# Kernel tuning notes

Hardware: AMD Instinct MI355X
Metric: run time of the kernel (lower is better)

Reference implementation:

```python
import jax, jax.numpy as jnp
import numpy as np
from jax import lax

# Model constants (match init_kwargs)
DIM = 512
NUM_HEADS = 8
HEAD_DIM = 64
INNER = NUM_HEADS * HEAD_DIM  # 512
SCALE = HEAD_DIM ** -0.5
# CoaT ConvRelPosEnc window dict {3:2, 5:3, 7:3}: head-group sizes and kernel sizes
HEAD_SPLITS = [2, 3, 3]
KSIZES = [3, 5, 7]


def _depthwise_conv(x, w, b):
    # x: [B, Cg, H, W], w: [Cg, 1, k, k] (OIHW, depthwise), b: [Cg]
    cg = x.shape[1]
    y = lax.conv_general_dilated(
        x, w, window_strides=(1, 1), padding='SAME',
        feature_group_count=cg,
        dimension_numbers=('NCHW', 'OIHW', 'NCHW'))
    return y + b[None, :, None, None]


def setup_inputs() -> dict:
    key = jax.random.key(0)
    ks = jax.random.split(key, 10)
    B, Himg, Wimg = 16, 56, 56
    N = Himg * Wimg
    x = jax.random.normal(ks[0], (B, N, DIM), dtype=jnp.float32)
    w_qkv = jax.random.normal(ks[1], (3 * INNER, DIM), dtype=jnp.float32) * 0.02
    w_proj = jax.random.normal(ks[2], (DIM, INNER), dtype=jnp.float32) * 0.02
    b_proj = jnp.zeros((DIM,), dtype=jnp.float32)
    # depthwise conv params per head group: channels = split * HEAD_DIM
    w3 = jax.random.normal(ks[3], (2 * HEAD_DIM, 1, 3, 3), dtype=jnp.float32) * 0.02
    b3 = jnp.zeros((2 * HEAD_DIM,), dtype=jnp.float32)
    w5 = jax.random.normal(ks[4], (3 * HEAD_DIM, 1, 5, 5), dtype=jnp.float32) * 0.02
    b5 = jnp.zeros((3 * HEAD_DIM,), dtype=jnp.float32)
    w7 = jax.random.normal(ks[5], (3 * HEAD_DIM, 1, 7, 7), dtype=jnp.float32) * 0.02
    b7 = jnp.zeros((3 * HEAD_DIM,), dtype=jnp.float32)
    return {"x": x, "H": Himg, "W": Wimg,
            "w_qkv": w_qkv, "w_proj": w_proj, "b_proj": b_proj,
            "w3": w3, "b3": b3, "w5": w5, "b5": b5, "w7": w7, "b7": b7}


def reference(x, H, W, w_qkv, w_proj, b_proj, w3, b3, w5, b5, w7, b7):
    B, N, C = x.shape
    h, d = NUM_HEADS, HEAD_DIM
    qkv = x @ w_qkv.T  # [B, N, 3*INNER]
    q, k, v = jnp.split(qkv, 3, axis=-1)
    # b n (h d) -> b h n d
    def to_heads(t):
        return t.reshape(B, N, h, d).transpose(0, 2, 1, 3)
    q, k, v = to_heads(q), to_heads(k), to_heads(v)
    # factorized attention: softmax(k) over sequence dim, then two batched GEMMs
    k_softmax = jax.nn.softmax(k, axis=2)
    kv = jnp.einsum('bhnk,bhnv->bhkv', k_softmax, v)          # [B,h,d,d]
    factor_att = jnp.einsum('bhnk,bhkv->bhnv', q, kv)          # [B,h,N,d]
    # ConvRelPosEnc: depthwise conv on v (as 2D map), elementwise multiply by q
    v_img = v.transpose(0, 1, 3, 2).reshape(B, h * d, H, W)    # [B, h*d, H, W]
    c0, c1 = HEAD_SPLITS[0] * d, (HEAD_SPLITS[0] + HEAD_SPLITS[1]) * d
    conv_v = jnp.concatenate([
        _depthwise_conv(v_img[:, :c0], w3, b3),
        _depthwise_conv(v_img[:, c0:c1], w5, b5),
        _depthwise_conv(v_img[:, c1:], w7, b7),
    ], axis=1)                                                 # [B, h*d, H, W]
    conv_v = conv_v.reshape(B, h, d, N).transpose(0, 1, 3, 2)  # [B,h,N,d]
    crpe = q * conv_v
    out = SCALE * factor_att + crpe                            # [B,h,N,d]
    out = out.transpose(0, 2, 1, 3).reshape(B, N, h * d)       # b h n d -> b n (h d)
    out = out @ w_proj.T + b_proj
    return out
```

## Files before the change

### kernel.cpp

```cpp
#include <hip/hip_runtime.h>
#include <hip/hip_bf16.h>
#include <cstdint>
#include <cstddef>

using u16 = unsigned short;
using u32 = unsigned int;
using f32x4 = __attribute__((ext_vector_type(4))) float;
using bf16x8 = __attribute__((ext_vector_type(8))) short;

#define NB   16
#define NSEQ 3136
#define NH   8
#define HD   64
#define CDIM 512
#define CQKV 1536

static __device__ __forceinline__ u16 f2bf(float f) {
  u32 u = __builtin_bit_cast(u32, f);
  u = (u + 0x7FFFu + ((u >> 16) & 1u)) >> 16;
  return (u16)u;
}
static __device__ __forceinline__ float bf2f(u16 h) {
  u32 u = ((u32)h) << 16;
  return __builtin_bit_cast(float, u);
}
static __device__ __forceinline__ void async16(const void* g, void* l) {
  __builtin_amdgcn_global_load_lds((const __attribute__((address_space(1))) u32*)g,
                                   (__attribute__((address_space(3))) u32*)l, 16, 0, 0);
}

__global__ __launch_bounds__(256) void cvt_kernel(const float* __restrict__ in,
                                                  u16* __restrict__ out, int n4) {
  int i = (int)(blockIdx.x * 256 + threadIdx.x);
  if (i >= n4) return;
  f32x4 v = *(const f32x4*)(in + (size_t)i * 4);
  uint2 uu;
  uu.x = (u32)f2bf(v[0]) | ((u32)f2bf(v[1]) << 16);
  uu.y = (u32)f2bf(v[2]) | ((u32)f2bf(v[3]) << 16);
  *(uint2*)(out + (size_t)i * 4) = uu;
}

#define VMW(n) asm volatile("s_waitcnt vmcnt(" #n ")" ::: "memory")

template<bool OUT_FP32>
__global__ __launch_bounds__(512, 2) void gemm256(
    const u16* __restrict__ Ap, const u16* __restrict__ Bp, void* __restrict__ Cp,
    const float* __restrict__ bias, int K, int lda, int ldb, int ldc, int nbn)
{
  __shared__ u16 sm[2][2][2][128 * 64];
  int nwg = (int)gridDim.x;
  int bid = (int)blockIdx.x;
  int wg = (bid & 7) * (nwg >> 3) + (bid >> 3);
  int bm = wg / nbn, bn = wg - bm * nbn;
  int m0 = bm * 256, n0 = bn * 256;
  int t = (int)threadIdx.x;
  int lane = t & 63, w = t >> 6;
  int wm = w >> 2, wn = w & 3;
  int lr = lane & 15, lk = (lane >> 4) * 8;

  f32x4 acc[2][2][4][2] = {};
  bf16x8 av[4][2], bv[2][2];
  const int KT = K >> 6;

  auto stage = [&](int b, int op, int half, int kt) {
    const u16* P = op ? Bp : Ap;
    int ld = op ? ldb : lda;
    int base0 = op ? n0 : m0;
    int gc = (kt << 6) + ((((t & 7) ^ ((t >> 3) & 7))) << 3);
    #pragma unroll
    for (int rd = 0; rd < 2; ++rd) {
      int gr = base0 + half * 128 + rd * 64 + (t >> 3);
      async16(P + (size_t)gr * ld + gc, &sm[b][op][half][rd * 4096 + w * 512]);
    }
  };
  auto LOADA = [&](int b, int h) {
    #pragma unroll
    for (int mi = 0; mi < 4; ++mi)
      #pragma unroll
      for (int kk = 0; kk < 2; ++kk) {
        int r = wm * 64 + mi * 16 + lr;
        int c = kk * 32 + lk;
        av[mi][kk] = *(const bf16x8*)&sm[b][0][h][r * 64 + (c ^ ((r & 7) << 3))];
      }
  };
  auto LOADB = [&](int b, int g) {
    #pragma unroll
    for (int ni = 0; ni < 2; ++ni)
      #pragma unroll
      for (int kk = 0; kk < 2; ++kk) {
        int r = wn * 32 + ni * 16 + lr;
        int c = kk * 32 + lk;
        bv[ni][kk] = *(const bf16x8*)&sm[b][1][g][r * 64 + (c ^ ((r & 7) << 3))];
      }
  };

#define BARSEQ                                                  \
  __builtin_amdgcn_s_barrier();                                 \
  asm volatile("s_waitcnt lgkmcnt(0)" ::: "memory");            \
  __builtin_amdgcn_sched_barrier(0);                            \
  __builtin_amdgcn_s_setprio(1)
#define ENDP                                                    \
  __builtin_amdgcn_s_setprio(0);                                \
  __builtin_amdgcn_s_barrier()
#define MMQ(h_, g_)                                                          \
  _Pragma("unroll")                                                          \
  for (int kk = 0; kk < 2; ++kk) {                                           \
    _Pragma("unroll")                                                        \
    for (int mi = 0; mi < 4; ++mi) {                                         \
      _Pragma("unroll")                                                      \
      for (int ni = 0; ni < 2; ++ni)                                         \
        acc[h_][g_][mi][ni] = __builtin_amdgcn_mfma_f32_16x16x32_bf16(       \
            av[mi][kk], bv[ni][kk], acc[h_][g_][mi][ni], 0, 0, 0);           \
    }                                                                        \
  }

  stage(0, 0, 0, 0); stage(0, 1, 0, 0); stage(0, 0, 1, 0); stage(0, 1, 1, 0);
  VMW(4);
  __builtin_amdgcn_s_barrier();

  for (int kt = 0; kt < KT - 1; ++kt) {
    int bb = kt & 1;
    LOADA(bb, 0); LOADB(bb, 0);
    stage(bb ^ 1, 0, 0, kt + 1);
    VMW(2);
    BARSEQ; MMQ(0, 0); ENDP;
    LOADB(bb, 1);
    stage(bb ^ 1, 1, 0, kt + 1);
    BARSEQ; MMQ(0, 1); ENDP;
    LOADA(bb, 1);
    stage(bb ^ 1, 0, 1, kt + 1);
    BARSEQ; MMQ(1, 1); ENDP;
    LOADB(bb, 0);
    stage(bb ^ 1, 1, 1, kt + 1);
    VMW(4);
    BARSEQ; MMQ(1, 0); ENDP;
  }
  {
    int bb = (KT - 1) & 1;
    LOADA(bb, 0); LOADB(bb, 0);
    VMW(0);
    BARSEQ; MMQ(0, 0); ENDP;
    LOADB(bb, 1);
    BARSEQ; MMQ(0, 1); ENDP;
    LOADA(bb, 1);
    BARSEQ; MMQ(1, 1); ENDP;
    LOADB(bb, 0);
    BARSEQ; MMQ(1, 0); ENDP;
  }
#undef MMQ
#undef BARSEQ
#undef ENDP

  if constexpr (!OUT_FP32) {
    __syncthreads();
    u16* cs = (u16*)sm;
    #pragma unroll
    for (int h = 0; h < 2; ++h)
      #pragma unroll
      for (int g = 0; g < 2; ++g)
        #pragma unroll
        for (int mi = 0; mi < 4; ++mi)
          #pragma unroll
          for (int ni = 0; ni < 2; ++ni)
            #pragma unroll
            for (int r = 0; r < 4; ++r) {
              int row = h * 128 + wm * 64 + mi * 16 + (lane >> 4) * 4 + r;
              int col = g * 128 + wn * 32 + ni * 16 + lr;
              cs[row * 256 + (col ^ (((row >> 2) & 7) << 3))] = f2bf(acc[h][g][mi][ni][r]);
            }
    __syncthreads();
    #pragma unroll
    for (int i = 0; i < 16; ++i) {
      int e = (i * 512 + t) * 8;
      int row = e >> 8, col = e & 255;
      uint4 v = *(const uint4*)&cs[row * 256 + (col ^ (((row >> 2) & 7) << 3))];
      *(uint4*)&((u16*)Cp)[(size_t)(m0 + row) * ldc + n0 + col] = v;
    }
  } else {
    float* cf = (float*)sm;
    #pragma unroll
    for (int h = 0; h < 2; ++h) {
      __syncthreads();
      #pragma unroll
      for (int g = 0; g < 2; ++g)
        #pragma unroll
        for (int mi = 0; mi < 4; ++mi)
          #pragma unroll
          for (int ni = 0; ni < 2; ++ni)
            #pragma unroll
            for (int r = 0; r < 4; ++r) {
              int row = wm * 64 + mi * 16 + (lane >> 4) * 4 + r;
              int col = g * 128 + wn * 32 + ni * 16 + lr;
              cf[row * 256 + (col ^ (((row >> 2) & 7) << 3))] = acc[h][g][mi][ni][r];
            }
      __syncthreads();
      #pragma unroll
      for (int i = 0; i < 16; ++i) {
        int e = (i * 512 + t) * 4;
        int row = e >> 8, col = e & 255;
        f32x4 v = *(const f32x4*)&cf[row * 256 + (col ^ (((row >> 2) & 7) << 3))];
        f32x4 b4 = *(const f32x4*)&bias[n0 + col];
        v += b4;
        *(f32x4*)&((float*)Cp)[(size_t)(m0 + h * 128 + row) * ldc + n0 + col] = v;
      }
    }
  }
}


static __device__ __forceinline__ void kvp_body(int bid, char* smem,
    const u16* __restrict__ qkvb, float* __restrict__ part) {
  int ns = bid & 7, h = (bid >> 3) & 7, b = bid >> 6;
  int t = (int)threadIdx.x;
  int lane = t & 63, w = t >> 6;
  u16* ekT = (u16*)smem;
  u16* vT  = (u16*)(smem + 8192);
  int nbase = ns * 392;
  int lr = lane & 15, lg = lane >> 4;
  f32x4 acc[4] = {};
  float sacc = 0.f;

  for (int tile = 0; tile < 7; ++tile) {
    __syncthreads();
    int lim = 392 - tile * 64;
    #pragma unroll
    for (int it = 0; it < 2; ++it) {
      int idx = it * 256 + t;
      int n = idx >> 3, c8 = idx & 7;
      uint4 kq; kq.x = 0u; kq.y = 0u; kq.z = 0u; kq.w = 0u;
      uint4 vq = kq;
      bool ok = (n < lim);
      if (ok) {
        size_t go = (size_t)(b * NSEQ + nbase + tile * 64 + n) * CQKV + h * HD + c8 * 8;
        kq = *(const uint4*)&qkvb[go + CDIM];
        vq = *(const uint4*)&qkvb[go + 2 * CDIM];
      }
      const u16* kp = (const u16*)&kq;
      const u16* vp = (const u16*)&vq;
      int pc = n ^ (c8 << 3);
      #pragma unroll
      for (int j = 0; j < 8; ++j) {
        int d = c8 * 8 + j;
        ekT[d * 64 + pc] = ok ? f2bf(__expf(bf2f(kp[j]))) : (u16)0;
        vT [d * 64 + pc] = vp[j];
      }
    }
    __syncthreads();
    bf16x8 av[2], bv[4][2];
    #pragma unroll
    for (int kk = 0; kk < 2; ++kk) {
      int r = w * 16 + lr;
      int c = kk * 32 + lg * 8;
      av[kk] = *(const bf16x8*)&ekT[r * 64 + (c ^ (((r >> 3) & 7) << 3))];
    }
    #pragma unroll
    for (int ni = 0; ni < 4; ++ni)
      #pragma unroll
      for (int kk = 0; kk < 2; ++kk) {
        int r = ni * 16 + lr;
        int c = kk * 32 + lg * 8;
        bv[ni][kk] = *(const bf16x8*)&vT[r * 64 + (c ^ (((r >> 3) & 7) << 3))];
      }
    #pragma unroll
    for (int kk = 0; kk < 2; ++kk)
      #pragma unroll
      for (int ni = 0; ni < 4; ++ni)
        acc[ni] = __builtin_amdgcn_mfma_f32_16x16x32_bf16(av[kk], bv[ni][kk], acc[ni], 0, 0, 0);
    {
      int r = w * 16 + lr;
      int c0 = lg * 16;
      int sw = (((r >> 3) & 7) << 3);
      bf16x8 s0 = *(const bf16x8*)&ekT[r * 64 + (c0 ^ sw)];
      bf16x8 s1 = *(const bf16x8*)&ekT[r * 64 + ((c0 + 8) ^ sw)];
      float ss = 0.f;
      #pragma unroll
      for (int j = 0; j < 8; ++j) ss += bf2f((u16)s0[j]) + bf2f((u16)s1[j]);
      sacc += ss;
    }
  }
  sacc += __shfl_xor(sacc, 16, 64);
  sacc += __shfl_xor(sacc, 32, 64);
  float* dst = part + (size_t)((ns * 16 + b) * 8 + h) * 4160;
  #pragma unroll
  for (int ni = 0; ni < 4; ++ni)
    #pragma unroll
    for (int r = 0; r < 4; ++r)
      dst[(w * 16 + lg * 4 + r) * 64 + ni * 16 + lr] = acc[ni][r];
  if (lane < 16) dst[4096 + w * 16 + lane] = sacc;
}

template<int R>
static __device__ __forceinline__ void conv_body(int bid, char* smem,
    const u16* __restrict__ qkvb, u16* __restrict__ cvout,
    const float* __restrict__ wp, const float* __restrict__ bias, int hbase, int nh) {
  constexpr int KS = 2 * R + 1;
  constexpr int WTY = 8 + 2 * R;
  constexpr int WTX = 14 + 2 * R;
  u16* vt = (u16*)smem;
  int hh = bid % nh;
  int tile = (bid / nh) % 28;
  int b = bid / (nh * 28);
  int h = hbase + hh;
  int y0 = (tile >> 2) * 8, x0 = (tile & 3) * 14;
  int t = (int)threadIdx.x;
  for (int idx = t; idx < WTY * WTX * 8; idx += 256) {
    int pix = idx >> 3, c8 = idx & 7;
    int py = pix / WTX, px = pix - py * WTX;
    int gy = y0 + py - R, gx = x0 + px - R;
    uint4 val; val.x = 0u; val.y = 0u; val.z = 0u; val.w = 0u;
    if (gy >= 0 && gy < 56 && gx >= 0 && gx < 56)
      val = *(const uint4*)&qkvb[(size_t)(b * NSEQ + gy * 56 + gx) * CQKV + 2 * CDIM + h * HD + c8 * 8];
    *(uint4*)&vt[pix * 64 + c8 * 8] = val;
  }
  __syncthreads();
  int d = t & 63, g = t >> 6;
  int cg = hh * 64 + d;
  float wr[KS * KS];
  #pragma unroll
  for (int i = 0; i < KS * KS; ++i) wr[i] = wp[cg * KS * KS + i];
  float bb = bias[cg];
  for (int px = g; px < 14; px += 4) {
    float acc[8];
    #pragma unroll
    for (int i = 0; i < 8; ++i) acc[i] = bb;
    #pragma unroll
    for (int iy = 0; iy < WTY; ++iy) {
      float val[KS];
      #pragma unroll
      for (int dx = 0; dx < KS; ++dx) val[dx] = bf2f(vt[(iy * WTX + px + dx) * 64 + d]);
      #pragma unroll
      for (int dy = 0; dy < KS; ++dy) {
        int py = iy - dy;
        if (py >= 0 && py < 8) {
          #pragma unroll
          for (int dx = 0; dx < KS; ++dx) acc[py] += wr[dy * KS + dx] * val[dx];
        }
      }
    }
    #pragma unroll
    for (int py = 0; py < 8; ++py)
      cvout[(size_t)(b * NSEQ + (y0 + py) * 56 + x0 + px) * CDIM + h * HD + d] = f2bf(acc[py]);
  }
}

__global__ __launch_bounds__(256) void mid_kernel(const u16* __restrict__ qkvb,
    u16* __restrict__ cvout, float* __restrict__ part,
    const float* __restrict__ w3, const float* __restrict__ b3,
    const float* __restrict__ w5, const float* __restrict__ b5,
    const float* __restrict__ w7, const float* __restrict__ b7) {
  __shared__ alignas(16) char smem[35840];
  int bid = (int)blockIdx.x;
  int q9 = bid / 9, r9 = bid - q9 * 9;
  if (r9 == 0 || r9 == 4) {
    kvp_body(q9 * 2 + (r9 == 4 ? 1 : 0), smem, qkvb, part);
  } else {
    int s = (r9 < 4) ? (r9 - 1) : (r9 - 2);
    int cid = q9 * 7 + s;
    if (cid < 896)        conv_body<1>(cid,        smem, qkvb, cvout, w3, b3, 0, 2);
    else if (cid < 2240)  conv_body<2>(cid - 896,  smem, qkvb, cvout, w5, b5, 2, 3);
    else                  conv_body<3>(cid - 2240, smem, qkvb, cvout, w7, b7, 5, 3);
  }
}

__global__ __launch_bounds__(256) void kv_reduce_kernel(const float* __restrict__ part,
                                                        float* __restrict__ kvb) {
  int idx = (int)(blockIdx.x * 256 + threadIdx.x);
  int bh = idx >> 10, e4 = idx & 1023;
  int b = bh >> 3, h = bh & 7;
  int dk = e4 >> 4;
  float s = 0.f;
  f32x4 o; o[0] = 0.f; o[1] = 0.f; o[2] = 0.f; o[3] = 0.f;
  #pragma unroll
  for (int c = 0; c < 8; ++c) {
    const float* src = part + (size_t)((c * 16 + b) * 8 + h) * 4160;
    o += *(const f32x4*)&src[e4 * 4];
    s += src[4096 + dk];
  }
  float inv = 1.0f / s;
  o *= inv;
  *(f32x4*)&kvb[(size_t)bh * 4096 + e4 * 4] = o;
}

__global__ __launch_bounds__(256) void combine_kernel(u16* __restrict__ qkvb,
                                                      const u16* __restrict__ cvin,
                                                      const float* __restrict__ kvb) {
  int bid = (int)blockIdx.x;
  int rt = bid % 49;
  int h = (bid / 49) & 7;
  int b = bid / 392;
  int n0 = rt * 64;
  int t = (int)threadIdx.x;
  int lane = t & 63, w = t >> 6;
  __shared__ u16 qs[64 * 72];
  __shared__ u16 cvs[64 * 64];
  __shared__ u16 kvT[64 * 64];

  #pragma unroll
  for (int i = 0; i < 2; ++i) {
    int idx = i * 256 + t;
    int row = idx >> 3, c8 = idx & 7;
    int srccol = (c8 ^ (row & 7)) << 3;
    async16(qkvb + (size_t)(b * NSEQ + n0 + row) * CQKV + h * HD + srccol, &qs[idx * 8]);
    async16(cvin + (size_t)(b * NSEQ + n0 + row) * CDIM + h * HD + srccol, &cvs[idx * 8]);
  }
  const float* kvsrc = kvb + (size_t)(b * 8 + h) * 4096;
  #pragma unroll
  for (int i = 0; i < 4; ++i) {
    int idx = i * 256 + t;
    int dk = idx & 63, dv0 = (idx >> 6) * 4;
    f32x4 v = *(const f32x4*)&kvsrc[dk * 64 + dv0];
    #pragma unroll
    for (int j = 0; j < 4; ++j) {
      int dv = dv0 + j;
      kvT[dv * 64 + ((((dk >> 3) ^ (dv & 7)) << 3) | (dk & 7))] = f2bf(v[j]);
    }
  }
  VMW(0);
  __syncthreads();

  int lr = lane & 15, lk = (lane >> 4) * 8;
  f32x4 acc[4] = {};
  bf16x8 av[2], bv[4][2];
  #pragma unroll
  for (int kk = 0; kk < 2; ++kk) {
    int r = w * 16 + lr;
    int c = kk * 32 + lk;
    av[kk] = *(const bf16x8*)&qs[r * 64 + (c ^ ((r & 7) << 3))];
  }
  #pragma unroll
  for (int ni = 0; ni < 4; ++ni)
    #pragma unroll
    for (int kk = 0; kk < 2; ++kk) {
      int r = ni * 16 + lr;
      int c = kk * 32 + lk;
      bv[ni][kk] = *(const bf16x8*)&kvT[r * 64 + (c ^ ((r & 7) << 3))];
    }
  #pragma unroll
  for (int kk = 0; kk < 2; ++kk)
    #pragma unroll
    for (int ni = 0; ni < 4; ++ni)
      acc[ni] = __builtin_amdgcn_mfma_f32_16x16x32_bf16(av[kk], bv[ni][kk], acc[ni], 0, 0, 0);

  float outv[4][4];
  #pragma unroll
  for (int ni = 0; ni < 4; ++ni)
    #pragma unroll
    for (int r = 0; r < 4; ++r) {
      int nrow = w * 16 + (lane >> 4) * 4 + r;
      int dv = ni * 16 + lr;
      int sw = ((((dv >> 3) ^ (nrow & 7)) << 3) | (dv & 7));
      float qv = bf2f(qs[nrow * 64 + sw]);
      float cv = bf2f(cvs[nrow * 64 + sw]);
      outv[ni][r] = 0.125f * acc[ni][r] + qv * cv;
    }
  __syncthreads();
  #pragma unroll
  for (int ni = 0; ni < 4; ++ni)
    #pragma unroll
    for (int r = 0; r < 4; ++r) {
      int nrow = w * 16 + (lane >> 4) * 4 + r;
      int dv = ni * 16 + lr;
      qs[nrow * 72 + dv] = f2bf(outv[ni][r]);
    }
  __syncthreads();
  {
    int row = t >> 2, c0 = (t & 3) * 16;
    uint4 x0 = *(const uint4*)&qs[row * 72 + c0];
    uint4 x1 = *(const uint4*)&qs[row * 72 + c0 + 8];
    u16* dst = &qkvb[(size_t)(b * NSEQ + n0 + row) * CQKV + h * HD + c0];
    *(uint4*)dst = x0;
    *(uint4*)&dst[8] = x1;
  }
}

extern "C" void kernel_launch(void* const* d_in, const int* in_sizes, int n_in,
                              void* d_out, int out_size, void* d_ws, size_t ws_size,
                              hipStream_t stream) {
  (void)in_sizes; (void)n_in; (void)out_size; (void)ws_size;
  const float* x      = (const float*)d_in[0];
  const float* w_qkv  = (const float*)d_in[3];
  const float* w_proj = (const float*)d_in[4];
  const float* b_proj = (const float*)d_in[5];
  const float* w3 = (const float*)d_in[6];
  const float* b3 = (const float*)d_in[7];
  const float* w5 = (const float*)d_in[8];
  const float* b5 = (const float*)d_in[9];
  const float* w7 = (const float*)d_in[10];
  const float* b7 = (const float*)d_in[11];
  float* out = (float*)d_out;

  char* ws = (char*)d_ws;
  u16* qkvb = (u16*)ws;        ws += (size_t)50176 * 1536 * 2;
  u16* wqb  = (u16*)ws;        ws += (size_t)1536 * 512 * 2;
  u16* wpb  = (u16*)ws;        ws += (size_t)512 * 512 * 2;
  float* kvpart = (float*)ws;  ws += (size_t)1024 * 4160 * 4;
  float* kvb = (float*)ws;     ws += (size_t)16 * 8 * 64 * 64 * 4;
  u16* xb = (u16*)ws;          ws += (size_t)50176 * 512 * 2;

  cvt_kernel<<<768, 256, 0, stream>>>(w_qkv, wqb, 1536 * 512 / 4);
  cvt_kernel<<<256, 256, 0, stream>>>(w_proj, wpb, 512 * 512 / 4);
  cvt_kernel<<<25088, 256, 0, stream>>>(x, xb, 50176 * 512 / 4);
  gemm256<false><<<1176, 512, 0, stream>>>(xb, wqb, qkvb, nullptr,
                                           512, 512, 512, 1536, 6);
  mid_kernel<<<4608, 256, 0, stream>>>(qkvb, xb, kvpart, w3, b3, w5, b5, w7, b7);
  kv_reduce_kernel<<<512, 256, 0, stream>>>(kvpart, kvb);
  combine_kernel<<<6272, 256, 0, stream>>>(qkvb, xb, kvb);
  gemm256<true><<<392, 512, 0, stream>>>(qkvb, wpb, out, b_proj,
                                         512, 1536, 512, 512, 2);
}
```

Before: 285.4 us.

## Transpose conv tile to channel-major shared layout and compute 2x14 outputs per thread

The depthwise-conv stage now stores the V tile in shared memory channel-major with padded rows (22 u16 per row), so each thread reads contiguous pixel rows for its channel as packed 32-bit pairs. Each thread now computes two output rows by fourteen columns, sharing every loaded input row between both output rows, where before it computed one column by eight rows. This cuts LDS reads and bf16 conversions per FMA. In exchange the scattered 2-byte LDS writes during the tile load may cause bank conflicts, register pressure rises from 28 accumulators plus up to 49 weights, and the shared buffer grows, which may lower occupancy.

```diff
diff --git a/kernel.cpp b/kernel.cpp
--- a/kernel.cpp
+++ b/kernel.cpp
@@ -296,6 +296,8 @@
   constexpr int KS = 2 * R + 1;
   constexpr int WTY = 8 + 2 * R;
   constexpr int WTX = 14 + 2 * R;
+  constexpr int RPAD = 22;
+  constexpr int ROWS = (R == 2) ? 13 : WTY;
   u16* vt = (u16*)smem;
   int hh = bid % nh;
   int tile = (bid / nh) % 28;
@@ -310,36 +312,58 @@
     uint4 val; val.x = 0u; val.y = 0u; val.z = 0u; val.w = 0u;
     if (gy >= 0 && gy < 56 && gx >= 0 && gx < 56)
       val = *(const uint4*)&qkvb[(size_t)(b * NSEQ + gy * 56 + gx) * CQKV + 2 * CDIM + h * HD + c8 * 8];
-    *(uint4*)&vt[pix * 64 + c8 * 8] = val;
+    const u16* vp = (const u16*)&val;
+    #pragma unroll
+    for (int j = 0; j < 8; ++j)
+      vt[(c8 * 8 + j) * (ROWS * RPAD) + py * RPAD + px] = vp[j];
   }
   __syncthreads();
   int d = t & 63, g = t >> 6;
   int cg = hh * 64 + d;
-  float wr[KS * KS];
-  #pragma unroll
-  for (int i = 0; i < KS * KS; ++i) wr[i] = wp[cg * KS * KS + i];
+  float w[KS * KS];
+  #pragma unroll
+  for (int i = 0; i < KS * KS; ++i) w[i] = wp[cg * KS * KS + i];
   float bb = bias[cg];
-  for (int px = g; px < 14; px += 4) {
-    float acc[8];
-    #pragma unroll
-    for (int i = 0; i < 8; ++i) acc[i] = bb;
-    #pragma unroll
-    for (int iy = 0; iy < WTY; ++iy) {
-      float val[KS];
-      #pragma unroll
-      for (int dx = 0; dx < KS; ++dx) val[dx] = bf2f(vt[(iy * WTX + px + dx) * 64 + d]);
-      #pragma unroll
-      for (int dy = 0; dy < KS; ++dy) {
-        int py = iy - dy;
-        if (py >= 0 && py < 8) {
-          #pragma unroll
-          for (int dx = 0; dx < KS; ++dx) acc[py] += wr[dy * KS + dx] * val[dx];
-        }
-      }
-    }
-    #pragma unroll
-    for (int py = 0; py < 8; ++py)
-      cvout[(size_t)(b * NSEQ + (y0 + py) * 56 + x0 + px) * CDIM + h * HD + d] = f2bf(acc[py]);
+  float acc[2][14];
+  #pragma unroll
+  for (int pp = 0; pp < 2; ++pp)
+    #pragma unroll
+    for (int px = 0; px < 14; ++px) acc[pp][px] = bb;
+  const u16* rowbase = &vt[d * (ROWS * RPAD)];
+  int py0 = g * 2;
+  #pragma unroll
+  for (int dy2 = 0; dy2 <= KS; ++dy2) {
+    float val[WTX];
+    const u32* rp = (const u32*)&rowbase[(py0 + dy2) * RPAD];
+    #pragma unroll
+    for (int c = 0; c < WTX / 2; ++c) {
+      u32 u = rp[c];
+      val[2 * c]     = __builtin_bit_cast(float, u << 16);
+      val[2 * c + 1] = __builtin_bit_cast(float, u & 0xffff0000u);
+    }
+    if (dy2 < KS) {
+      #pragma unroll
+      for (int dx = 0; dx < KS; ++dx) {
+        float wv = w[dy2 * KS + dx];
+        #pragma unroll
+        for (int px = 0; px < 14; ++px) acc[0][px] += wv * val[px + dx];
+      }
+    }
+    if (dy2 >= 1) {
+      #pragma unroll
+      for (int dx = 0; dx < KS; ++dx) {
+        float wv = w[(dy2 - 1) * KS + dx];
+        #pragma unroll
+        for (int px = 0; px < 14; ++px) acc[1][px] += wv * val[px + dx];
+      }
+    }
+  }
+  #pragma unroll
+  for (int pp = 0; pp < 2; ++pp) {
+    int py = py0 + pp;
+    #pragma unroll
+    for (int px = 0; px < 14; ++px)
+      cvout[(size_t)(b * NSEQ + (y0 + py) * 56 + x0 + px) * CDIM + h * HD + d] = f2bf(acc[pp][px]);
   }
 }
 
@@ -348,7 +372,7 @@
     const float* __restrict__ w3, const float* __restrict__ b3,
     const float* __restrict__ w5, const float* __restrict__ b5,
     const float* __restrict__ w7, const float* __restrict__ b7) {
-  __shared__ alignas(16) char smem[35840];
+  __shared__ alignas(16) char smem[39424];
   int bid = (int)blockIdx.x;
   int q9 = bid / 9, r9 = bid - q9 * 9;
   if (r9 == 0 || r9 == 4) {
```

Measured after the change: 296.7 us. 1.04x slower.

## Make QKV GEMM persistent and prefetch next tile during epilogue

Applied to the files above, without the earlier changes.

The QKV projection GEMM becomes a persistent kernel. A 256-block grid loops over all 1176 output tiles. During the last K step of each tile it stages the first K slice of the next tile into the free shared-memory buffer. It then writes the bf16 epilogue through the other buffer in two halves, so the prefetch overlaps the store. The goal is to hide per-tile prologue and launch tail cost, at the expense of running only one block per CU and uneven tile counts per block.

```diff
diff --git a/kernel.cpp b/kernel.cpp
--- a/kernel.cpp
+++ b/kernel.cpp
@@ -28,6 +28,11 @@
   __builtin_amdgcn_global_load_lds((const __attribute__((address_space(1))) u32*)g,
                                    (__attribute__((address_space(3))) u32*)l, 16, 0, 0);
 }
+
+#define VMW(n) asm volatile("s_waitcnt vmcnt(" #n ")" ::: "memory")
+#define LGKM0BAR                                                \
+  asm volatile("s_waitcnt lgkmcnt(0)" ::: "memory");            \
+  __builtin_amdgcn_s_barrier()
 
 __global__ __launch_bounds__(256) void cvt_kernel(const float* __restrict__ in,
                                                   u16* __restrict__ out, int n4) {
@@ -40,32 +45,26 @@
   *(uint2*)(out + (size_t)i * 4) = uu;
 }
 
-#define VMW(n) asm volatile("s_waitcnt vmcnt(" #n ")" ::: "memory")
-
 template<bool OUT_FP32>
 __global__ __launch_bounds__(512, 2) void gemm256(
     const u16* __restrict__ Ap, const u16* __restrict__ Bp, void* __restrict__ Cp,
-    const float* __restrict__ bias, int K, int lda, int ldb, int ldc, int nbn)
+    const float* __restrict__ bias, int K, int lda, int ldb, int ldc, int nbn, int ntotal)
 {
   __shared__ u16 sm[2][2][2][128 * 64];
-  int nwg = (int)gridDim.x;
-  int bid = (int)blockIdx.x;
-  int wg = (bid & 7) * (nwg >> 3) + (bid >> 3);
-  int bm = wg / nbn, bn = wg - bm * nbn;
-  int m0 = bm * 256, n0 = bn * 256;
   int t = (int)threadIdx.x;
   int lane = t & 63, w = t >> 6;
   int wm = w >> 2, wn = w & 3;
   int lr = lane & 15, lk = (lane >> 4) * 8;
-
-  f32x4 acc[2][2][4][2] = {};
+  const int KT = K >> 6;
+  int grid = (int)gridDim.x;
+  int nper = ntotal >> 3;
+
   bf16x8 av[4][2], bv[2][2];
-  const int KT = K >> 6;
-
-  auto stage = [&](int b, int op, int half, int kt) {
+
+  auto stage = [&](int b, int op, int half, int kt, int bm0, int bn0) {
     const u16* P = op ? Bp : Ap;
     int ld = op ? ldb : lda;
-    int base0 = op ? n0 : m0;
+    int base0 = op ? bn0 : bm0;
     int gc = (kt << 6) + ((((t & 7) ^ ((t >> 3) & 7))) << 3);
     #pragma unroll
     for (int rd = 0; rd < 2; ++rd) {
@@ -93,6 +92,27 @@
         bv[ni][kk] = *(const bf16x8*)&sm[b][1][g][r * 64 + (c ^ ((r & 7) << 3))];
       }
   };
+
+  int raw = (int)blockIdx.x;
+  int wg = (raw & 7) * nper + (raw >> 3);
+  int bm = wg / nbn, bn = wg - bm * nbn;
+  int m0 = bm * 256, n0 = bn * 256;
+
+  stage(0, 0, 0, 0, m0, n0); stage(0, 1, 0, 0, m0, n0);
+  stage(0, 0, 1, 0, m0, n0); stage(0, 1, 1, 0, m0, n0);
+  VMW(4);
+  __builtin_amdgcn_s_barrier();
+
+  while (true) {
+    f32x4 acc[2][2][4][2] = {};
+    int nraw = raw + grid;
+    bool has_next = (nraw < ntotal);
+    int nm0 = 0, nn0 = 0;
+    if (has_next) {
+      int nwg2 = (nraw & 7) * nper + (nraw >> 3);
+      int nbm = nwg2 / nbn, nbn2 = nwg2 - nbm * nbn;
+      nm0 = nbm * 256; nn0 = nbn2 * 256;
+    }
 
 #define BARSEQ                                                  \
   __builtin_amdgcn_s_barrier();                                 \
@@ -114,96 +134,114 @@
     }                                                                        \
   }
 
-  stage(0, 0, 0, 0); stage(0, 1, 0, 0); stage(0, 0, 1, 0); stage(0, 1, 1, 0);
-  VMW(4);
-  __builtin_amdgcn_s_barrier();
-
-  for (int kt = 0; kt < KT - 1; ++kt) {
-    int bb = kt & 1;
-    LOADA(bb, 0); LOADB(bb, 0);
-    stage(bb ^ 1, 0, 0, kt + 1);
-    VMW(2);
-    BARSEQ; MMQ(0, 0); ENDP;
-    LOADB(bb, 1);
-    stage(bb ^ 1, 1, 0, kt + 1);
-    BARSEQ; MMQ(0, 1); ENDP;
-    LOADA(bb, 1);
-    stage(bb ^ 1, 0, 1, kt + 1);
-    BARSEQ; MMQ(1, 1); ENDP;
-    LOADB(bb, 0);
-    stage(bb ^ 1, 1, 1, kt + 1);
-    VMW(4);
-    BARSEQ; MMQ(1, 0); ENDP;
-  }
-  {
-    int bb = (KT - 1) & 1;
-    LOADA(bb, 0); LOADB(bb, 0);
-    VMW(0);
-    BARSEQ; MMQ(0, 0); ENDP;
-    LOADB(bb, 1);
-    BARSEQ; MMQ(0, 1); ENDP;
-    LOADA(bb, 1);
-    BARSEQ; MMQ(1, 1); ENDP;
-    LOADB(bb, 0);
-    BARSEQ; MMQ(1, 0); ENDP;
-  }
+    for (int kt = 0; kt < KT - 1; ++kt) {
+      int bb = kt & 1;
+      LOADA(bb, 0); LOADB(bb, 0);
+      stage(bb ^ 1, 0, 0, kt + 1, m0, n0);
+      VMW(2);
+      BARSEQ; MMQ(0, 0); ENDP;
+      LOADB(bb, 1);
+      stage(bb ^ 1, 1, 0, kt + 1, m0, n0);
+      BARSEQ; MMQ(0, 1); ENDP;
+      LOADA(bb, 1);
+      stage(bb ^ 1, 0, 1, kt + 1, m0, n0);
+      BARSEQ; MMQ(1, 1); ENDP;
+      LOADB(bb, 0);
+      stage(bb ^ 1, 1, 1, kt + 1, m0, n0);
+      VMW(4);
+      BARSEQ; MMQ(1, 0); ENDP;
+    }
+    {
+      int bb = (KT - 1) & 1;
+      if (has_next) {
+        LOADA(bb, 0); LOADB(bb, 0);
+        stage(bb ^ 1, 0, 0, 0, nm0, nn0);
+        VMW(2);
+        BARSEQ; MMQ(0, 0); ENDP;
+        LOADB(bb, 1);
+        stage(bb ^ 1, 1, 0, 0, nm0, nn0);
+        BARSEQ; MMQ(0, 1); ENDP;
+        LOADA(bb, 1);
+        stage(bb ^ 1, 0, 1, 0, nm0, nn0);
+        BARSEQ; MMQ(1, 1); ENDP;
+        LOADB(bb, 0);
+        stage(bb ^ 1, 1, 1, 0, nm0, nn0);
+        VMW(4);
+        BARSEQ; MMQ(1, 0); ENDP;
+      } else {
+        LOADA(bb, 0); LOADB(bb, 0);
+        VMW(0);
+        BARSEQ; MMQ(0, 0); ENDP;
+        LOADB(bb, 1);
+        BARSEQ; MMQ(0, 1); ENDP;
+        LOADA(bb, 1);
+        BARSEQ; MMQ(1, 1); ENDP;
+        LOADB(bb, 0);
+        BARSEQ; MMQ(1, 0); ENDP;
+      }
+    }
 #undef MMQ
 #undef BARSEQ
 #undef ENDP
 
-  if constexpr (!OUT_FP32) {
-    __syncthreads();
-    u16* cs = (u16*)sm;
-    #pragma unroll
-    for (int h = 0; h < 2; ++h)
-      #pragma unroll
-      for (int g = 0; g < 2; ++g)
+    if constexpr (!OUT_FP32) {
+      u16* cs = (u16*)&sm[1][0][0][0];
+      #pragma unroll
+      for (int h = 0; h < 2; ++h) {
+        LGKM0BAR;
         #pragma unroll
-        for (int mi = 0; mi < 4; ++mi)
+        for (int g = 0; g < 2; ++g)
           #pragma unroll
-          for (int ni = 0; ni < 2; ++ni)
+          for (int mi = 0; mi < 4; ++mi)
             #pragma unroll
-            for (int r = 0; r < 4; ++r) {
-              int row = h * 128 + wm * 64 + mi * 16 + (lane >> 4) * 4 + r;
-              int col = g * 128 + wn * 32 + ni * 16 + lr;
-              cs[row * 256 + (col ^ (((row >> 2) & 7) << 3))] = f2bf(acc[h][g][mi][ni][r]);
-            }
-    __syncthreads();
-    #pragma unroll
-    for (int i = 0; i < 16; ++i) {
-      int e = (i * 512 + t) * 8;
-      int row = e >> 8, col = e & 255;
-      uint4 v = *(const uint4*)&cs[row * 256 + (col ^ (((row >> 2) & 7) << 3))];
-      *(uint4*)&((u16*)Cp)[(size_t)(m0 + row) * ldc + n0 + col] = v;
-    }
-  } else {
-    float* cf = (float*)sm;
-    #pragma unroll
-    for (int h = 0; h < 2; ++h) {
-      __syncthreads();
-      #pragma unroll
-      for (int g = 0; g < 2; ++g)
+            for (int ni = 0; ni < 2; ++ni)
+              #pragma unroll
+              for (int r = 0; r < 4; ++r) {
+                int row = wm * 64 + mi * 16 + (lane >> 4) * 4 + r;
+                int col = g * 128 + wn * 32 + ni * 16 + lr;
+                cs[row * 256 + (col ^ (((row >> 2) & 7) << 3))] = f2bf(acc[h][g][mi][ni][r]);
+              }
+        LGKM0BAR;
         #pragma unroll
-        for (int mi = 0; mi < 4; ++mi)
+        for (int i = 0; i < 8; ++i) {
+          int e = (i * 512 + t) * 8;
+          int row = e >> 8, col = e & 255;
+          uint4 v = *(const uint4*)&cs[row * 256 + (col ^ (((row >> 2) & 7) << 3))];
+          *(uint4*)&((u16*)Cp)[(size_t)(m0 + h * 128 + row) * ldc + n0 + col] = v;
+        }
+      }
+    } else {
+      float* cf = (float*)sm;
+      #pragma unroll
+      for (int h = 0; h < 2; ++h) {
+        LGKM0BAR;
+        #pragma unroll
+        for (int g = 0; g < 2; ++g)
           #pragma unroll
-          for (int ni = 0; ni < 2; ++ni)
+          for (int mi = 0; mi < 4; ++mi)
             #pragma unroll
-            for (int r = 0; r < 4; ++r) {
-              int row = wm * 64 + mi * 16 + (lane >> 4) * 4 + r;
-              int col = g * 128 + wn * 32 + ni * 16 + lr;
-              cf[row * 256 + (col ^ (((row >> 2) & 7) << 3))] = acc[h][g][mi][ni][r];
-            }
-      __syncthreads();
-      #pragma unroll
-      for (int i = 0; i < 16; ++i) {
-        int e = (i * 512 + t) * 4;
-        int row = e >> 8, col = e & 255;
-        f32x4 v = *(const f32x4*)&cf[row * 256 + (col ^ (((row >> 2) & 7) << 3))];
-        f32x4 b4 = *(const f32x4*)&bias[n0 + col];
-        v += b4;
-        *(f32x4*)&((float*)Cp)[(size_t)(m0 + h * 128 + row) * ldc + n0 + col] = v;
-      }
-    }
+            for (int ni = 0; ni < 2; ++ni)
+              #pragma unroll
+              for (int r = 0; r < 4; ++r) {
+                int row = wm * 64 + mi * 16 + (lane >> 4) * 4 + r;
+                int col = g * 128 + wn * 32 + ni * 16 + lr;
+                cf[row * 256 + (col ^ (((row >> 2) & 7) << 3))] = acc[h][g][mi][ni][r];
+              }
+        LGKM0BAR;
+        #pragma unroll
+        for (int i = 0; i < 16; ++i) {
+          int e = (i * 512 + t) * 4;
+          int row = e >> 8, col = e & 255;
+          f32x4 v = *(const f32x4*)&cf[row * 256 + (col ^ (((row >> 2) & 7) << 3))];
+          f32x4 b4 = *(const f32x4*)&bias[n0 + col];
+          v += b4;
+          *(f32x4*)&((float*)Cp)[(size_t)(m0 + h * 128 + row) * ldc + n0 + col] = v;
+        }
+      }
+    }
+    if (!has_next) break;
+    LGKM0BAR;
+    raw = nraw; m0 = nm0; n0 = nn0;
   }
 }
 
@@ -500,11 +538,11 @@
   cvt_kernel<<<768, 256, 0, stream>>>(w_qkv, wqb, 1536 * 512 / 4);
   cvt_kernel<<<256, 256, 0, stream>>>(w_proj, wpb, 512 * 512 / 4);
   cvt_kernel<<<25088, 256, 0, stream>>>(x, xb, 50176 * 512 / 4);
-  gemm256<false><<<1176, 512, 0, stream>>>(xb, wqb, qkvb, nullptr,
-                                           512, 512, 512, 1536, 6);
+  gemm256<false><<<256, 512, 0, stream>>>(xb, wqb, qkvb, nullptr,
+                                          512, 512, 512, 1536, 6, 1176);
   mid_kernel<<<4608, 256, 0, stream>>>(qkvb, xb, kvpart, w3, b3, w5, b5, w7, b7);
   kv_reduce_kernel<<<512, 256, 0, stream>>>(kvpart, kvb);
   combine_kernel<<<6272, 256, 0, stream>>>(qkvb, xb, kvb);
   gemm256<true><<<392, 512, 0, stream>>>(qkvb, wpb, out, b_proj,
-                                         512, 1536, 512, 512, 2);
-}
+                                         512, 1536, 512, 512, 2, 392);
+}
```

Measured after the change: 448.7 us. 1.57x slower.
